# Kernel tuning notes

Hardware: AMD Instinct MI355X
Metric: run time of the kernel (lower is better)

## Reference

```python
import jax, jax.numpy as jnp
import numpy as np

B, S, D, H = 4, 1024, 1024, 16
DK = D // H


def setup_inputs() -> dict:
    key = jax.random.key(0)
    ks = jax.random.split(key, 14)
    scale = 1.0 / np.sqrt(D)
    inp = {
        "Qx": jax.random.normal(ks[0], (B, S, D), jnp.float32),
        "Kx": jax.random.normal(ks[1], (B, S, D), jnp.float32),
        "Vx": jax.random.normal(ks[2], (B, S, D), jnp.float32),
        "prob_phn": jax.random.uniform(ks[3], (B, S, S), jnp.float32),
        "mask": jax.random.randint(ks[4], (B, S, S), 0, 2, jnp.int32),
        "lambda_val": 1,
        "Wq": jax.random.normal(ks[5], (D, D), jnp.float32) * scale,
        "bq": jnp.zeros((D,), jnp.float32),
        "Wk": jax.random.normal(ks[6], (D, D), jnp.float32) * scale,
        "bk": jnp.zeros((D,), jnp.float32),
        "Wv": jax.random.normal(ks[7], (D, D), jnp.float32) * scale,
        "bv": jnp.zeros((D,), jnp.float32),
        "Wo": jax.random.normal(ks[8], (D, D), jnp.float32) * scale,
        "bo": jnp.zeros((D,), jnp.float32),
    }
    return inp


def _split_heads(x):
    # [B,S,D] -> [B,H,S,DK]
    b, s, _ = x.shape
    return x.reshape(b, s, H, DK).transpose(0, 2, 1, 3)


def reference(Qx, Kx, Vx, prob_phn, mask, lambda_val, Wq, bq, Wk, bk, Wv, bv, Wo, bo):
    q = _split_heads(Qx @ Wq.T + bq)
    k = _split_heads(Kx @ Wk.T + bk)
    v = _split_heads(Vx @ Wv.T + bv)
    scores = jnp.einsum("bhqd,bhkd->bhqk", q, k) / jnp.sqrt(jnp.float32(DK))
    if lambda_val > 0:
        # prob_phn: [B,S,S] -> transpose last two dims, broadcast over heads
        scores = scores - lambda_val * jnp.swapaxes(prob_phn, -2, -1)[:, None]
    scores = jnp.where(mask[:, None] == 0, jnp.float32(-1e9), scores)
    probs = jax.nn.softmax(scores, axis=-1)
    attn = jnp.einsum("bhqk,bhkd->bhqd", probs, v)
    out = attn.transpose(0, 2, 1, 3).reshape(Qx.shape[0], Qx.shape[1], D)
    out = out @ Wo.T + bo
    return (out, mask)
```

## Files before the change

### kernel.cpp

```cpp
#include <hip/hip_runtime.h>
#include <hip/hip_bf16.h>
#include <cstdint>
#include <cstddef>

#define BB 4
#define SS 1024
#define DD 1024
#define HH 16
#define DKK 64

typedef unsigned short u16;
typedef __bf16 bf16_t;
typedef __attribute__((ext_vector_type(8))) bf16_t bf16x8;
typedef __attribute__((ext_vector_type(4))) float floatx4;

#define LOG2E 1.4426950408889634f
#define QKSCALE 0.18033688011112042f

static __device__ inline u16 f2bf(float f) {
    union { float f; unsigned u; } v; v.f = f;
    unsigned r = v.u + 0x7fffu + ((v.u >> 16) & 1u);
    return (u16)(r >> 16);
}

static __device__ inline void load16_lds(const void* g, void* l) {
    __builtin_amdgcn_global_load_lds(
        (const __attribute__((address_space(1))) unsigned int*)g,
        (__attribute__((address_space(3))) unsigned int*)l,
        16, 0, 0);
}

static __device__ inline int swz64(int row, int c) { return row * 64 + ((c ^ (row & 7)) * 8); }
static __device__ inline int swz32(int row, int c) { return row * 32 + ((c ^ ((row >> 1) & 3)) * 8); }

static __device__ inline float lam_val(const int* p) {
    int v = *p;
    if (v >= -100000 && v <= 100000) return (float)v;
    union { int i; float f; } u; u.i = v; return u.f;
}

__global__ void prep_kernel(const float* __restrict__ Qx, const float* __restrict__ Kx,
                            const float* __restrict__ Vx,
                            const float* __restrict__ Wq, const float* __restrict__ Wk,
                            const float* __restrict__ Wv, const float* __restrict__ Wo,
                            const float* __restrict__ prob, const int* __restrict__ mask,
                            const int* __restrict__ lam_p,
                            u16* __restrict__ Xq, u16* __restrict__ Xk, u16* __restrict__ Xv,
                            u16* __restrict__ wq, u16* __restrict__ wk,
                            u16* __restrict__ wv, u16* __restrict__ wo,
                            u16* __restrict__ biasB, float* __restrict__ maskOut)
{
    __shared__ float tile[64][65];
    const int blk = blockIdx.x, tid = threadIdx.x;

    if (blk >= 1024) {
        const int cb = blk - 1024;
        const int base = cb * 1024;
        const float* src; u16* dst; int off0;
        if (base < 3145728) {
            int s = base >> 20;  off0 = base & 1048575;
            src = (s == 0) ? Qx : (s == 1) ? Kx : Vx;
            dst = (s == 0) ? Xq : (s == 1) ? Xk : Xv;
        } else {
            int v2 = base - 3145728;
            int s = v2 >> 18;  off0 = v2 & 262143;
            src = (s == 0) ? Wq : (s == 1) ? Wk : (s == 2) ? Wv : Wo;
            dst = (s == 0) ? wq : (s == 1) ? wk : (s == 2) ? wv : wo;
        }
        float4 f[4];
        #pragma unroll
        for (int r = 0; r < 4; ++r)
            f[r] = ((const float4*)src)[off0 + r * 256 + tid];
        #pragma unroll
        for (int r = 0; r < 4; ++r) {
            ushort4 o;
            o.x = f2bf(f[r].x); o.y = f2bf(f[r].y);
            o.z = f2bf(f[r].z); o.w = f2bf(f[r].w);
            ((ushort4*)dst)[off0 + r * 256 + tid] = o;
        }
        return;
    }

    const int b = blk >> 8;
    const int q0 = ((blk >> 4) & 15) * 64, k0 = (blk & 15) * 64;
    #pragma unroll
    for (int rr = 0; rr < 4; ++rr) {
        int unit = rr * 256 + tid;
        int kl = unit >> 4, qi = unit & 15;
        float4 p4 = *(const float4*)&prob[((size_t)(b * SS + k0 + kl)) * SS + q0 + qi * 4];
        tile[kl][qi * 4 + 0] = p4.x;
        tile[kl][qi * 4 + 1] = p4.y;
        tile[kl][qi * 4 + 2] = p4.z;
        tile[kl][qi * 4 + 3] = p4.w;
    }
    __syncthreads();
    const float lamс = lam_val(lam_p) * LOG2E;
    #pragma unroll
    for (int rr = 0; rr < 4; ++rr) {
        int pair = rr * 256 + tid;
        int q = pair >> 4, k4 = pair & 15;
        size_t oidx = ((size_t)(b * SS + q0 + q)) * SS + k0 + k4 * 4;
        int4 m4 = *(const int4*)&mask[oidx];
        float p0 = tile[k4 * 4 + 0][q];
        float p1 = tile[k4 * 4 + 1][q];
        float p2 = tile[k4 * 4 + 2][q];
        float p3 = tile[k4 * 4 + 3][q];
        ushort4 bb;
        bb.x = f2bf((m4.x == 0) ? -1.5e9f : -lamс * p0);
        bb.y = f2bf((m4.y == 0) ? -1.5e9f : -lamс * p1);
        bb.z = f2bf((m4.z == 0) ? -1.5e9f : -lamс * p2);
        bb.w = f2bf((m4.w == 0) ? -1.5e9f : -lamс * p3);
        *(ushort4*)&biasB[oidx] = bb;
        if (maskOut) {
            float4 mf = { (float)m4.x, (float)m4.y, (float)m4.z, (float)m4.w };
            *(float4*)&maskOut[oidx] = mf;
        }
    }
}

template <int MODE>
static __device__ inline void gemm_body(const u16* __restrict__ A, const u16* __restrict__ W,
                                        const float* __restrict__ bias,
                                        u16* __restrict__ Cb, float* __restrict__ Cf)
{
    constexpr int K = 1024, N = 1024;
    __shared__ __align__(16) u16 As[128 * 32];
    __shared__ __align__(16) u16 Bs[128 * 32];
    const int tid = threadIdx.x;
    const int wv = tid >> 6, ln = tid & 63, l15 = ln & 15, quad = ln >> 4;
    const int mBase = blockIdx.y * 128;
    const int nBase = blockIdx.x * 128;
    const int wm = (wv & 1) * 64, wn = (wv >> 1) * 64;

    const u16* Aptr[2]; const u16* Wptr[2];
    #pragma unroll
    for (int r = 0; r < 2; ++r) {
        int p = r * 256 + wv * 64 + ln;
        int row = p >> 2;
        int c = (p & 3) ^ ((row >> 1) & 3);
        Aptr[r] = A + (size_t)(mBase + row) * K + c * 8;
        Wptr[r] = W + (size_t)(nBase + row) * K + c * 8;
    }

    floatx4 acc[4][4] = {};

    for (int k0 = 0; k0 < K; k0 += 32) {
        __syncthreads();
        #pragma unroll
        for (int r = 0; r < 2; ++r) {
            load16_lds(Aptr[r] + k0, &As[(r * 256 + wv * 64) * 8]);
            load16_lds(Wptr[r] + k0, &Bs[(r * 256 + wv * 64) * 8]);
        }
        __syncthreads();
        bf16x8 af[4], bfr[4];
        #pragma unroll
        for (int i = 0; i < 4; ++i)
            af[i] = *(const bf16x8*)&As[swz32(wm + i * 16 + l15, quad)];
        #pragma unroll
        for (int j = 0; j < 4; ++j)
            bfr[j] = *(const bf16x8*)&Bs[swz32(wn + j * 16 + l15, quad)];
        #pragma unroll
        for (int i = 0; i < 4; ++i)
            #pragma unroll
            for (int j = 0; j < 4; ++j)
                acc[i][j] = __builtin_amdgcn_mfma_f32_16x16x32_bf16(af[i], bfr[j], acc[i][j], 0, 0, 0);
    }

    #pragma unroll
    for (int i = 0; i < 4; ++i) {
        #pragma unroll
        for (int j = 0; j < 4; ++j) {
            int col = nBase + wn + j * 16 + l15;
            float bcol = bias[col];
            if (MODE == 2) {
                int hh = col >> 6, dk = col & 63;
                int row0 = mBase + wm + i * 16 + quad * 4;
                int bb = row0 >> 10, s = row0 & 1023;
                ushort4 v4;
                v4.x = f2bf(acc[i][j][0] + bcol);
                v4.y = f2bf(acc[i][j][1] + bcol);
                v4.z = f2bf(acc[i][j][2] + bcol);
                v4.w = f2bf(acc[i][j][3] + bcol);
                *(ushort4*)&Cb[((size_t)((bb * HH + hh) * DKK) + dk) * SS + s] = v4;
            } else {
                #pragma unroll
                for (int r = 0; r < 4; ++r) {
                    int row = mBase + wm + i * 16 + quad * 4 + r;
                    float v = acc[i][j][r] + bcol;
                    if (MODE == 1) Cf[(size_t)row * N + col] = v;
                    else           Cb[(size_t)row * N + col] = f2bf(v);
                }
            }
        }
    }
}

__global__ __launch_bounds__(256) void gemm_qkv_kernel(
    const u16* __restrict__ Xq, const u16* __restrict__ Xk, const u16* __restrict__ Xv,
    const u16* __restrict__ Wq, const u16* __restrict__ Wk, const u16* __restrict__ Wv,
    const float* __restrict__ bq, const float* __restrict__ bk, const float* __restrict__ bv,
    u16* __restrict__ Cq, u16* __restrict__ Ck, u16* __restrict__ Vtout)
{
    const int z = blockIdx.z;
    if (z == 2) {
        gemm_body<2>(Xv, Wv, bv, Vtout, nullptr);
    } else {
        const u16* A = (z == 0) ? Xq : Xk;
        const u16* W = (z == 0) ? Wq : Wk;
        const float* bias = (z == 0) ? bq : bk;
        u16* C = (z == 0) ? Cq : Ck;
        gemm_body<0>(A, W, bias, C, nullptr);
    }
}

__global__ __launch_bounds__(256) void gemm_out_kernel(
    const u16* __restrict__ A, const u16* __restrict__ W,
    const float* __restrict__ bias, float* __restrict__ Cf)
{
    gemm_body<1>(A, W, bias, nullptr, Cf);
}

__global__ __launch_bounds__(256) void attn_kernel(
    const u16* __restrict__ Qf, const u16* __restrict__ Kf,
    const u16* __restrict__ Vt, const u16* __restrict__ biasB,
    u16* __restrict__ Attn)
{
    __shared__ __align__(16) u16 Qs[64 * 64];
    __shared__ __align__(16) u16 Ks[64 * 64];
    __shared__ __align__(16) u16 Vs[64 * 64];
    __shared__ __align__(16) u16 Ps[4][16 * 72];
    __shared__ float Rs[4][16];
    const int tid = threadIdx.x;
    const int wv = tid >> 6, ln = tid & 63, l15 = ln & 15, quad = ln >> 4;
    const int qt = blockIdx.x, h = blockIdx.y, b = blockIdx.z;
    const int q0 = qt * 64;

    int row64[2], col64[2];
    #pragma unroll
    for (int r = 0; r < 2; ++r) {
        int p = r * 256 + wv * 64 + ln;
        row64[r] = p >> 3;
        col64[r] = ((p & 7) ^ (row64[r] & 7)) * 8;
    }

    #pragma unroll
    for (int r = 0; r < 2; ++r)
        load16_lds(Qf + ((size_t)(b * SS + q0 + row64[r])) * DD + h * DKK + col64[r],
                   &Qs[(r * 256 + wv * 64) * 8]);
    __syncthreads();

    bf16x8 aq[2];
    #pragma unroll
    for (int t = 0; t < 2; ++t)
        aq[t] = *(const bf16x8*)&Qs[swz64(wv * 16 + l15, t * 4 + quad)];

    const size_t vt_head = ((size_t)(b * HH + h)) * DKK * SS;
    const u16* Kp[2]; const u16* Vp[2];
    #pragma unroll
    for (int r = 0; r < 2; ++r) {
        Kp[r] = Kf + ((size_t)(b * SS + row64[r])) * DD + h * DKK + col64[r];
        Vp[r] = Vt + vt_head + (size_t)row64[r] * SS + col64[r];
    }

    const u16* bp = biasB + ((size_t)(b * SS + q0 + wv * 16 + l15)) * SS + quad * 4;

    floatx4 o[4] = {};
    float rsum = 0.f;

    for (int kt = 0; kt < 16; ++kt) {
        const int kk0 = kt * 64;
        __syncthreads();
        #pragma unroll
        for (int r = 0; r < 2; ++r) {
            load16_lds(Kp[r] + (size_t)kk0 * DD, &Ks[(r * 256 + wv * 64) * 8]);
            load16_lds(Vp[r] + kk0, &Vs[(r * 256 + wv * 64) * 8]);
        }
        __syncthreads();

        uint2 braw[4];
        #pragma unroll
        for (int j = 0; j < 4; ++j)
            braw[j] = *(const uint2*)&bp[kk0 + j * 16];

        floatx4 sfr[4];
        #pragma unroll
        for (int j = 0; j < 4; ++j) {
            bf16x8 bk0 = *(const bf16x8*)&Ks[swz64(j * 16 + l15, quad)];
            bf16x8 bk1 = *(const bf16x8*)&Ks[swz64(j * 16 + l15, 4 + quad)];
            floatx4 s = {};
            s = __builtin_amdgcn_mfma_f32_16x16x32_bf16(bk0, aq[0], s, 0, 0, 0);
            sfr[j] = __builtin_amdgcn_mfma_f32_16x16x32_bf16(bk1, aq[1], s, 0, 0, 0);
        }

        #pragma unroll
        for (int j = 0; j < 4; ++j) {
            float b0 = __uint_as_float(braw[j].x << 16);
            float b1 = __uint_as_float(braw[j].x & 0xffff0000u);
            float b2 = __uint_as_float(braw[j].y << 16);
            float b3 = __uint_as_float(braw[j].y & 0xffff0000u);
            float p0 = __builtin_amdgcn_exp2f(fmaf(sfr[j][0], QKSCALE, b0));
            float p1 = __builtin_amdgcn_exp2f(fmaf(sfr[j][1], QKSCALE, b1));
            float p2 = __builtin_amdgcn_exp2f(fmaf(sfr[j][2], QKSCALE, b2));
            float p3 = __builtin_amdgcn_exp2f(fmaf(sfr[j][3], QKSCALE, b3));
            rsum += (p0 + p1) + (p2 + p3);
            uint2 pk;
            pk.x = (__float_as_uint(p0) >> 16) | (__float_as_uint(p1) & 0xffff0000u);
            pk.y = (__float_as_uint(p2) >> 16) | (__float_as_uint(p3) & 0xffff0000u);
            *(uint2*)&Ps[wv][l15 * 72 + j * 16 + quad * 4] = pk;
        }

        #pragma unroll
        for (int t = 0; t < 2; ++t) {
            bf16x8 ap = *(const bf16x8*)&Ps[wv][l15 * 72 + t * 32 + quad * 8];
            #pragma unroll
            for (int j = 0; j < 4; ++j) {
                bf16x8 bvv = *(const bf16x8*)&Vs[swz64(j * 16 + l15, t * 4 + quad)];
                o[j] = __builtin_amdgcn_mfma_f32_16x16x32_bf16(ap, bvv, o[j], 0, 0, 0);
            }
        }
    }

    rsum += __shfl_xor(rsum, 16);
    rsum += __shfl_xor(rsum, 32);
    if (ln < 16) Rs[wv][l15] = 1.0f / rsum;
    float4 rv = *(const float4*)&Rs[wv][quad * 4];

    #pragma unroll
    for (int j = 0; j < 4; ++j) {
        #pragma unroll
        for (int r = 0; r < 4; ++r) {
            int srow = q0 + wv * 16 + quad * 4 + r;
            int dk = j * 16 + l15;
            float ri = (r == 0) ? rv.x : (r == 1) ? rv.y : (r == 2) ? rv.z : rv.w;
            Attn[((size_t)(b * SS + srow)) * DD + h * DKK + dk] = f2bf(o[j][r] * ri);
        }
    }
}

extern "C" void kernel_launch(void* const* d_in, const int* in_sizes, int n_in,
                              void* d_out, int out_size, void* d_ws, size_t ws_size,
                              hipStream_t stream)
{
    const float* Qx  = (const float*)d_in[0];
    const float* Kx  = (const float*)d_in[1];
    const float* Vx  = (const float*)d_in[2];
    const float* prob = (const float*)d_in[3];
    const int*   mask = (const int*)d_in[4];
    const int*   lam  = (const int*)d_in[5];
    const float* Wq  = (const float*)d_in[6];
    const float* bq  = (const float*)d_in[7];
    const float* Wk  = (const float*)d_in[8];
    const float* bk  = (const float*)d_in[9];
    const float* Wv  = (const float*)d_in[10];
    const float* bv  = (const float*)d_in[11];
    const float* Wo  = (const float*)d_in[12];
    const float* bo  = (const float*)d_in[13];

    char* ws = (char*)d_ws;
    const size_t MB = 1024 * 1024;
    u16*   Xq     = (u16*)(ws + 0 * MB);
    u16*   Xk     = (u16*)(ws + 8 * MB);
    u16*   Xv     = (u16*)(ws + 16 * MB);
    u16*   wq     = (u16*)(ws + 24 * MB);
    u16*   wk     = (u16*)(ws + 26 * MB);
    u16*   wvp    = (u16*)(ws + 28 * MB);
    u16*   wo     = (u16*)(ws + 30 * MB);
    u16*   q_flat = (u16*)(ws + 32 * MB);
    u16*   k_flat = (u16*)(ws + 40 * MB);
    u16*   vt     = (u16*)(ws + 56 * MB);
    u16*   biasB  = (u16*)(ws + 64 * MB);
    u16*   attn   = (u16*)(ws + 80 * MB);

    float* maskOut = (out_size >= 2 * BB * SS * DD) ? (float*)d_out + (size_t)BB * SS * DD
                                                    : nullptr;

    prep_kernel<<<5120, 256, 0, stream>>>(Qx, Kx, Vx, Wq, Wk, Wv, Wo, prob, mask, lam,
                                          Xq, Xk, Xv, wq, wk, wvp, wo, biasB, maskOut);
    gemm_qkv_kernel<<<dim3(8, 32, 3), 256, 0, stream>>>(Xq, Xk, Xv, wq, wk, wvp,
                                                        bq, bk, bv, q_flat, k_flat, vt);
    attn_kernel<<<dim3(16, 16, 4), 256, 0, stream>>>(q_flat, k_flat, vt, biasB, attn);
    gemm_out_kernel<<<dim3(8, 32, 1), 256, 0, stream>>>(attn, wo, bo, (float*)d_out);
}
```

Before: 264.2 us.

## Double-buffer K/V tiles and prefetch bias in attention kernel

Attention kernel now keeps two LDS buffers for the K and V tiles. It issues the loads for tile kt+1, along with the bias values for the next step, before computing on tile kt, and needs one barrier per iteration instead of two. The aim is to hide global-load latency behind the MFMA and softmax work. The cost is double LDS for K/V, which may reduce occupancy, plus more registers for the prefetched bias. A Cyrillic-character variable name is also renamed.

```diff
diff --git a/kernel.cpp b/kernel.cpp
--- a/kernel.cpp
+++ b/kernel.cpp
@@ -94,7 +94,7 @@
         tile[kl][qi * 4 + 3] = p4.w;
     }
     __syncthreads();
-    const float lamс = lam_val(lam_p) * LOG2E;
+    const float lamc = lam_val(lam_p) * LOG2E;
     #pragma unroll
     for (int rr = 0; rr < 4; ++rr) {
         int pair = rr * 256 + tid;
@@ -106,10 +106,10 @@
         float p2 = tile[k4 * 4 + 2][q];
         float p3 = tile[k4 * 4 + 3][q];
         ushort4 bb;
-        bb.x = f2bf((m4.x == 0) ? -1.5e9f : -lamс * p0);
-        bb.y = f2bf((m4.y == 0) ? -1.5e9f : -lamс * p1);
-        bb.z = f2bf((m4.z == 0) ? -1.5e9f : -lamс * p2);
-        bb.w = f2bf((m4.w == 0) ? -1.5e9f : -lamс * p3);
+        bb.x = f2bf((m4.x == 0) ? -1.5e9f : -lamc * p0);
+        bb.y = f2bf((m4.y == 0) ? -1.5e9f : -lamc * p1);
+        bb.z = f2bf((m4.z == 0) ? -1.5e9f : -lamc * p2);
+        bb.w = f2bf((m4.w == 0) ? -1.5e9f : -lamc * p3);
         *(ushort4*)&biasB[oidx] = bb;
         if (maskOut) {
             float4 mf = { (float)m4.x, (float)m4.y, (float)m4.z, (float)m4.w };
@@ -226,8 +226,8 @@
     u16* __restrict__ Attn)
 {
     __shared__ __align__(16) u16 Qs[64 * 64];
-    __shared__ __align__(16) u16 Ks[64 * 64];
-    __shared__ __align__(16) u16 Vs[64 * 64];
+    __shared__ __align__(16) u16 Ks[2][64 * 64];
+    __shared__ __align__(16) u16 Vs[2][64 * 64];
     __shared__ __align__(16) u16 Ps[4][16 * 72];
     __shared__ float Rs[4][16];
     const int tid = threadIdx.x;
@@ -243,17 +243,6 @@
         col64[r] = ((p & 7) ^ (row64[r] & 7)) * 8;
     }
 
-    #pragma unroll
-    for (int r = 0; r < 2; ++r)
-        load16_lds(Qf + ((size_t)(b * SS + q0 + row64[r])) * DD + h * DKK + col64[r],
-                   &Qs[(r * 256 + wv * 64) * 8]);
-    __syncthreads();
-
-    bf16x8 aq[2];
-    #pragma unroll
-    for (int t = 0; t < 2; ++t)
-        aq[t] = *(const bf16x8*)&Qs[swz64(wv * 16 + l15, t * 4 + quad)];
-
     const size_t vt_head = ((size_t)(b * HH + h)) * DKK * SS;
     const u16* Kp[2]; const u16* Vp[2];
     #pragma unroll
@@ -262,31 +251,52 @@
         Vp[r] = Vt + vt_head + (size_t)row64[r] * SS + col64[r];
     }
 
+    #pragma unroll
+    for (int r = 0; r < 2; ++r) {
+        load16_lds(Qf + ((size_t)(b * SS + q0 + row64[r])) * DD + h * DKK + col64[r],
+                   &Qs[(r * 256 + wv * 64) * 8]);
+        load16_lds(Kp[r], &Ks[0][(r * 256 + wv * 64) * 8]);
+        load16_lds(Vp[r], &Vs[0][(r * 256 + wv * 64) * 8]);
+    }
+
     const u16* bp = biasB + ((size_t)(b * SS + q0 + wv * 16 + l15)) * SS + quad * 4;
+    uint2 braw[4];
+    #pragma unroll
+    for (int j = 0; j < 4; ++j)
+        braw[j] = *(const uint2*)&bp[j * 16];
+
+    __syncthreads();
+
+    bf16x8 aq[2];
+    #pragma unroll
+    for (int t = 0; t < 2; ++t)
+        aq[t] = *(const bf16x8*)&Qs[swz64(wv * 16 + l15, t * 4 + quad)];
 
     floatx4 o[4] = {};
     float rsum = 0.f;
+    int cur = 0;
 
     for (int kt = 0; kt < 16; ++kt) {
-        const int kk0 = kt * 64;
-        __syncthreads();
-        #pragma unroll
-        for (int r = 0; r < 2; ++r) {
-            load16_lds(Kp[r] + (size_t)kk0 * DD, &Ks[(r * 256 + wv * 64) * 8]);
-            load16_lds(Vp[r] + kk0, &Vs[(r * 256 + wv * 64) * 8]);
-        }
-        __syncthreads();
-
-        uint2 braw[4];
-        #pragma unroll
-        for (int j = 0; j < 4; ++j)
-            braw[j] = *(const uint2*)&bp[kk0 + j * 16];
+        const int nxt = cur ^ 1;
+
+        uint2 bnext[4];
+        if (kt < 15) {
+            const int kk1 = (kt + 1) * 64;
+            #pragma unroll
+            for (int r = 0; r < 2; ++r) {
+                load16_lds(Kp[r] + (size_t)kk1 * DD, &Ks[nxt][(r * 256 + wv * 64) * 8]);
+                load16_lds(Vp[r] + kk1, &Vs[nxt][(r * 256 + wv * 64) * 8]);
+            }
+            #pragma unroll
+            for (int j = 0; j < 4; ++j)
+                bnext[j] = *(const uint2*)&bp[kk1 + j * 16];
+        }
 
         floatx4 sfr[4];
         #pragma unroll
         for (int j = 0; j < 4; ++j) {
-            bf16x8 bk0 = *(const bf16x8*)&Ks[swz64(j * 16 + l15, quad)];
-            bf16x8 bk1 = *(const bf16x8*)&Ks[swz64(j * 16 + l15, 4 + quad)];
+            bf16x8 bk0 = *(const bf16x8*)&Ks[cur][swz64(j * 16 + l15, quad)];
+            bf16x8 bk1 = *(const bf16x8*)&Ks[cur][swz64(j * 16 + l15, 4 + quad)];
             floatx4 s = {};
             s = __builtin_amdgcn_mfma_f32_16x16x32_bf16(bk0, aq[0], s, 0, 0, 0);
             sfr[j] = __builtin_amdgcn_mfma_f32_16x16x32_bf16(bk1, aq[1], s, 0, 0, 0);
@@ -314,10 +324,18 @@
             bf16x8 ap = *(const bf16x8*)&Ps[wv][l15 * 72 + t * 32 + quad * 8];
             #pragma unroll
             for (int j = 0; j < 4; ++j) {
-                bf16x8 bvv = *(const bf16x8*)&Vs[swz64(j * 16 + l15, t * 4 + quad)];
+                bf16x8 bvv = *(const bf16x8*)&Vs[cur][swz64(j * 16 + l15, t * 4 + quad)];
                 o[j] = __builtin_amdgcn_mfma_f32_16x16x32_bf16(ap, bvv, o[j], 0, 0, 0);
             }
         }
+
+        if (kt < 15) {
+            #pragma unroll
+            for (int j = 0; j < 4; ++j)
+                braw[j] = bnext[j];
+            __syncthreads();
+        }
+        cur = nxt;
     }
 
     rsum += __shfl_xor(rsum, 16);
```

New measurement: 290.0 us. 1.1x slower.

## Load V fragments directly to registers, swizzle block order, raise occupancy bound

Applied to the files above, without the earlier changes.

The attention kernel stops staging V through shared memory. Each wave now reads its V^T MFMA operands straight from global memory into registers, which removes the Vs buffer and its LDS reads. Blocks are remapped with a linear-index swizzle so that consecutively scheduled blocks spread across heads and batches, and launch_bounds asks for 5 blocks per SM. The catch is that every wave now loads the full V tile itself, so global and L2 traffic rises, and the tighter occupancy target may squeeze registers. It also renames a variable that held a non-ASCII character.

```diff
diff --git a/kernel.cpp b/kernel.cpp
--- a/kernel.cpp
+++ b/kernel.cpp
@@ -94,7 +94,7 @@
         tile[kl][qi * 4 + 3] = p4.w;
     }
     __syncthreads();
-    const float lamс = lam_val(lam_p) * LOG2E;
+    const float lamc = lam_val(lam_p) * LOG2E;
     #pragma unroll
     for (int rr = 0; rr < 4; ++rr) {
         int pair = rr * 256 + tid;
@@ -106,10 +106,10 @@
         float p2 = tile[k4 * 4 + 2][q];
         float p3 = tile[k4 * 4 + 3][q];
         ushort4 bb;
-        bb.x = f2bf((m4.x == 0) ? -1.5e9f : -lamс * p0);
-        bb.y = f2bf((m4.y == 0) ? -1.5e9f : -lamс * p1);
-        bb.z = f2bf((m4.z == 0) ? -1.5e9f : -lamс * p2);
-        bb.w = f2bf((m4.w == 0) ? -1.5e9f : -lamс * p3);
+        bb.x = f2bf((m4.x == 0) ? -1.5e9f : -lamc * p0);
+        bb.y = f2bf((m4.y == 0) ? -1.5e9f : -lamc * p1);
+        bb.z = f2bf((m4.z == 0) ? -1.5e9f : -lamc * p2);
+        bb.w = f2bf((m4.w == 0) ? -1.5e9f : -lamc * p3);
         *(ushort4*)&biasB[oidx] = bb;
         if (maskOut) {
             float4 mf = { (float)m4.x, (float)m4.y, (float)m4.z, (float)m4.w };
@@ -220,19 +220,21 @@
     gemm_body<1>(A, W, bias, nullptr, Cf);
 }
 
-__global__ __launch_bounds__(256) void attn_kernel(
+__global__ __launch_bounds__(256, 5) void attn_kernel(
     const u16* __restrict__ Qf, const u16* __restrict__ Kf,
     const u16* __restrict__ Vt, const u16* __restrict__ biasB,
     u16* __restrict__ Attn)
 {
     __shared__ __align__(16) u16 Qs[64 * 64];
     __shared__ __align__(16) u16 Ks[64 * 64];
-    __shared__ __align__(16) u16 Vs[64 * 64];
     __shared__ __align__(16) u16 Ps[4][16 * 72];
     __shared__ float Rs[4][16];
     const int tid = threadIdx.x;
     const int wv = tid >> 6, ln = tid & 63, l15 = ln & 15, quad = ln >> 4;
-    const int qt = blockIdx.x, h = blockIdx.y, b = blockIdx.z;
+
+    const int lin = blockIdx.x + 16 * blockIdx.y + 256 * blockIdx.z;
+    const int sw  = (lin & 7) * 128 + (lin >> 3);
+    const int qt = sw & 15, h = (sw >> 4) & 15, b = sw >> 8;
     const int q0 = qt * 64;
 
     int row64[2], col64[2];
@@ -254,13 +256,16 @@
     for (int t = 0; t < 2; ++t)
         aq[t] = *(const bf16x8*)&Qs[swz64(wv * 16 + l15, t * 4 + quad)];
 
+    const u16* Kp[2];
+    #pragma unroll
+    for (int r = 0; r < 2; ++r)
+        Kp[r] = Kf + ((size_t)(b * SS + row64[r])) * DD + h * DKK + col64[r];
+
     const size_t vt_head = ((size_t)(b * HH + h)) * DKK * SS;
-    const u16* Kp[2]; const u16* Vp[2];
-    #pragma unroll
-    for (int r = 0; r < 2; ++r) {
-        Kp[r] = Kf + ((size_t)(b * SS + row64[r])) * DD + h * DKK + col64[r];
-        Vp[r] = Vt + vt_head + (size_t)row64[r] * SS + col64[r];
-    }
+    const u16* vrow[4];
+    #pragma unroll
+    for (int j = 0; j < 4; ++j)
+        vrow[j] = Vt + vt_head + (size_t)(j * 16 + l15) * SS + quad * 8;
 
     const u16* bp = biasB + ((size_t)(b * SS + q0 + wv * 16 + l15)) * SS + quad * 4;
 
@@ -270,17 +275,24 @@
     for (int kt = 0; kt < 16; ++kt) {
         const int kk0 = kt * 64;
         __syncthreads();
-        #pragma unroll
-        for (int r = 0; r < 2; ++r) {
+
+        #pragma unroll
+        for (int r = 0; r < 2; ++r)
             load16_lds(Kp[r] + (size_t)kk0 * DD, &Ks[(r * 256 + wv * 64) * 8]);
-            load16_lds(Vp[r] + kk0, &Vs[(r * 256 + wv * 64) * 8]);
-        }
-        __syncthreads();
+
+        bf16x8 vf[2][4];
+        #pragma unroll
+        for (int t = 0; t < 2; ++t)
+            #pragma unroll
+            for (int j = 0; j < 4; ++j)
+                vf[t][j] = *(const bf16x8*)&vrow[j][kk0 + t * 32];
 
         uint2 braw[4];
         #pragma unroll
         for (int j = 0; j < 4; ++j)
             braw[j] = *(const uint2*)&bp[kk0 + j * 16];
+
+        __syncthreads();
 
         floatx4 sfr[4];
         #pragma unroll
@@ -313,10 +325,8 @@
         for (int t = 0; t < 2; ++t) {
             bf16x8 ap = *(const bf16x8*)&Ps[wv][l15 * 72 + t * 32 + quad * 8];
             #pragma unroll
-            for (int j = 0; j < 4; ++j) {
-                bf16x8 bvv = *(const bf16x8*)&Vs[swz64(j * 16 + l15, t * 4 + quad)];
-                o[j] = __builtin_amdgcn_mfma_f32_16x16x32_bf16(ap, bvv, o[j], 0, 0, 0);
-            }
+            for (int j = 0; j < 4; ++j)
+                o[j] = __builtin_amdgcn_mfma_f32_16x16x32_bf16(ap, vf[t][j], o[j], 0, 0, 0);
         }
     }
 
```

After: 319.7 us. 1.21x slower.
